# Kernel optimization log

Hardware: AMD Instinct MI355X
Metric: run time of the kernel (lower is better)

Reference implementation:

```python
import jax, jax.numpy as jnp
import numpy as np

# bitsandbytes NF4 codebook (16 quantile values in [-1, 1])
NF4 = jnp.array([
    -1.0, -0.6961928009986877, -0.5250730514526367, -0.39491748809814453,
    -0.28444138169288635, -0.18477343022823334, -0.09105003625154495, 0.0,
    0.07958029955625534, 0.16093020141124725, 0.24611230194568634,
    0.33791524171829224, 0.44070982933044434, 0.5626170039176941,
    0.7229568362236328, 1.0], dtype=jnp.float32)
BLOCK = 64  # bnb default quantization blocksize


def dequant_nf4(codes, absmax):
    """codes: int array of 4-bit indices, absmax: per-64-elem-block scale."""
    flat = NF4[codes.reshape(-1)]                      # codebook lookup
    flat = flat.reshape(-1, BLOCK) * absmax[:, None]   # per-block rescale
    return flat.reshape(codes.shape)


def setup_inputs() -> dict:
    key = jax.random.key(0)
    k1, k2, k3, k4, k5 = jax.random.split(key, 5)
    B, S, IN, OUT, R = 4, 2048, 4096, 4096, 8
    x = jax.random.normal(k1, (B, S, IN), dtype=jnp.float32)
    codes_A = jax.random.randint(k2, (R, IN), 0, 16, dtype=jnp.int32)
    absmax_A = jax.random.uniform(k3, (R * IN // BLOCK,), dtype=jnp.float32)
    codes_B = jax.random.randint(k4, (OUT, R), 0, 16, dtype=jnp.int32)
    absmax_B = jax.random.uniform(k5, (OUT * R // BLOCK,), dtype=jnp.float32)
    return {"x": x, "codes_A": codes_A, "absmax_A": absmax_A,
            "codes_B": codes_B, "absmax_B": absmax_B}


def reference(x, codes_A, absmax_A, codes_B, absmax_B):
    SCALING = 32.0 / 8.0  # alpha / rank
    W_A = dequant_nf4(codes_A, absmax_A)   # [rank, in]
    W_B = dequant_nf4(codes_B, absmax_B)   # [out, rank]
    interm = jnp.einsum('bsi,ri->bsr', x, W_A)          # lora_A: x @ W_A^T
    out = jnp.einsum('bsr,or->bso', interm, W_B)        # lora_B
    return out * SCALING
```

## Files before the change

kernel.cpp:

```cpp
#include <hip/hip_runtime.h>


static __device__ __constant__ float NF4_TBL[16] = {
    -1.0f, -0.6961928009986877f, -0.5250730514526367f, -0.39491748809814453f,
    -0.28444138169288635f, -0.18477343022823334f, -0.09105003625154495f, 0.0f,
    0.07958029955625534f, 0.16093020141124725f, 0.24611230194568634f,
    0.33791524171829224f, 0.44070982933044434f, 0.5626170039176941f,
    0.7229568362236328f, 1.0f};

__global__ void nf4_dequant_kernel(const int* __restrict__ codesA,
                                   const float* __restrict__ absA,
                                   const int* __restrict__ codesB,
                                   const float* __restrict__ absB,
                                   float* __restrict__ wA,
                                   float* __restrict__ wBt,
                                   int n) {
    int id = blockIdx.x * blockDim.x + threadIdx.x;
    if (id < n) {
        wA[id] = NF4_TBL[codesA[id] & 15] * absA[id >> 6];
        const int r = id >> 12;
        const int o = id & 4095;
        wBt[id] = NF4_TBL[codesB[o * 8 + r] & 15] * absB[o >> 3];
    }
}

__global__ __launch_bounds__(256) void lora_fused_kernel(
    const float* __restrict__ x,
    const float* __restrict__ wA,
    const float* __restrict__ wBt,
    float* __restrict__ out) {
    __shared__ float p_s[4][4][8];
    __shared__ float im_s[4][8];

    const int t    = threadIdx.x;
    const int wave = t >> 6;
    const int lane = t & 63;
    const int g    = lane >> 4;
    const int l16  = lane & 15;
    const int row0 = blockIdx.x * 4;

    const float4* __restrict__ xg =
        (const float4*)(x + (size_t)(row0 + g) * 4096) + wave * 256;
    const float4* __restrict__ wq = (const float4*)wA + wave * 256;

    float acc[8];
    #pragma unroll
    for (int r = 0; r < 8; ++r) acc[r] = 0.f;

    #pragma unroll 4
    for (int s = 0; s < 16; ++s) {
        const int idx = s * 16 + l16;
        const float4 xa = xg[idx];
        #pragma unroll
        for (int r = 0; r < 8; ++r) {
            const float4 w = wq[r * 1024 + idx];
            acc[r] += xa.x * w.x + xa.y * w.y + xa.z * w.z + xa.w * w.w;
        }
    }

    #pragma unroll
    for (int r = 0; r < 8; ++r) {
        float v = acc[r];
        #pragma unroll
        for (int off = 8; off > 0; off >>= 1) v += __shfl_down(v, off, 16);
        if (l16 == 0) p_s[wave][g][r] = v;
    }
    __syncthreads();

    if (t < 32) {
        const int m = t >> 3, r = t & 7;
        im_s[m][r] = (p_s[0][m][r] + p_s[1][m][r] +
                      p_s[2][m][r] + p_s[3][m][r]) * 4.0f;
    }
    __syncthreads();

    float ims[4][8];
    #pragma unroll
    for (int m = 0; m < 4; ++m)
        #pragma unroll
        for (int r = 0; r < 8; ++r)
            ims[m][r] = __int_as_float(
                __builtin_amdgcn_readfirstlane(__float_as_int(im_s[m][r])));

    const float4* __restrict__ wt = (const float4*)wBt;

    #pragma unroll 1
    for (int k = 0; k < 4; ++k) {
        const int og = t + 256 * k;
        float4 w[8];
        #pragma unroll
        for (int r = 0; r < 8; ++r) w[r] = wt[r * 1024 + og];

        #pragma unroll
        for (int m = 0; m < 4; ++m) {
            float4 s;
            s.x = ims[m][0] * w[0].x + ims[m][1] * w[1].x + ims[m][2] * w[2].x
                + ims[m][3] * w[3].x + ims[m][4] * w[4].x + ims[m][5] * w[5].x
                + ims[m][6] * w[6].x + ims[m][7] * w[7].x;
            s.y = ims[m][0] * w[0].y + ims[m][1] * w[1].y + ims[m][2] * w[2].y
                + ims[m][3] * w[3].y + ims[m][4] * w[4].y + ims[m][5] * w[5].y
                + ims[m][6] * w[6].y + ims[m][7] * w[7].y;
            s.z = ims[m][0] * w[0].z + ims[m][1] * w[1].z + ims[m][2] * w[2].z
                + ims[m][3] * w[3].z + ims[m][4] * w[4].z + ims[m][5] * w[5].z
                + ims[m][6] * w[6].z + ims[m][7] * w[7].z;
            s.w = ims[m][0] * w[0].w + ims[m][1] * w[1].w + ims[m][2] * w[2].w
                + ims[m][3] * w[3].w + ims[m][4] * w[4].w + ims[m][5] * w[5].w
                + ims[m][6] * w[6].w + ims[m][7] * w[7].w;
            ((float4*)(out + (size_t)(row0 + m) * 4096))[og] = s;
        }
    }
}

extern "C" void kernel_launch(void* const* d_in, const int* in_sizes, int n_in,
                              void* d_out, int out_size, void* d_ws, size_t ws_size,
                              hipStream_t stream) {
    const float* x        = (const float*)d_in[0];
    const int*   codes_A  = (const int*)d_in[1];
    const float* absmax_A = (const float*)d_in[2];
    const int*   codes_B  = (const int*)d_in[3];
    const float* absmax_B = (const float*)d_in[4];
    float* out = (float*)d_out;

    constexpr int NW = 8 * 4096;
    float* wA  = (float*)d_ws;
    float* wBt = (float*)d_ws + NW;

    nf4_dequant_kernel<<<(NW + 255) / 256, 256, 0, stream>>>(
        codes_A, absmax_A, codes_B, absmax_B, wA, wBt, NW);

    lora_fused_kernel<<<8192 / 4, 256, 0, stream>>>(x, wA, wBt, out);
}
```

Measured before the change: 268.0 us.

## Assign four rows per wave to reuse W_A loads and drop shared-memory reduction

Each wave now handles four full rows instead of the block splitting four rows across waves, so every W_A float4 load is reused across four rows. The cross-wave shared-memory reduction and the two __syncthreads are replaced by a full-wave shuffle reduction. The grid shrinks from 2048 to 512 blocks, which lowers parallelism and raises register pressure because of the 32 accumulators, while cutting redundant W_A and W_B traffic per row.

```diff
diff --git a/kernel.cpp b/kernel.cpp
--- a/kernel.cpp
+++ b/kernel.cpp
@@ -29,64 +29,61 @@
     const float* __restrict__ wA,
     const float* __restrict__ wBt,
     float* __restrict__ out) {
-    __shared__ float p_s[4][4][8];
-    __shared__ float im_s[4][8];
+    const int lane = threadIdx.x & 63;
+    const int wid  = blockIdx.x * 4 + (threadIdx.x >> 6);
+    const size_t row0 = (size_t)wid * 4;
 
-    const int t    = threadIdx.x;
-    const int wave = t >> 6;
-    const int lane = t & 63;
-    const int g    = lane >> 4;
-    const int l16  = lane & 15;
-    const int row0 = blockIdx.x * 4;
+    const float4* __restrict__ x0  = (const float4*)(x + row0 * 4096);
+    const float4* __restrict__ x1  = x0 + 1024;
+    const float4* __restrict__ x2  = x0 + 2048;
+    const float4* __restrict__ x3  = x0 + 3072;
+    const float4* __restrict__ wA4 = (const float4*)wA;
 
-    const float4* __restrict__ xg =
-        (const float4*)(x + (size_t)(row0 + g) * 4096) + wave * 256;
-    const float4* __restrict__ wq = (const float4*)wA + wave * 256;
+    float acc[4][8];
+    #pragma unroll
+    for (int m = 0; m < 4; ++m)
+        #pragma unroll
+        for (int r = 0; r < 8; ++r) acc[m][r] = 0.f;
 
-    float acc[8];
-    #pragma unroll
-    for (int r = 0; r < 8; ++r) acc[r] = 0.f;
-
-    #pragma unroll 4
-    for (int s = 0; s < 16; ++s) {
-        const int idx = s * 16 + l16;
-        const float4 xa = xg[idx];
+    #pragma unroll 1
+    for (int q = 0; q < 16; ++q) {
+        const int idx = q * 64 + lane;
+        const float4 a0 = x0[idx];
+        const float4 a1 = x1[idx];
+        const float4 a2 = x2[idx];
+        const float4 a3 = x3[idx];
         #pragma unroll
         for (int r = 0; r < 8; ++r) {
-            const float4 w = wq[r * 1024 + idx];
-            acc[r] += xa.x * w.x + xa.y * w.y + xa.z * w.z + xa.w * w.w;
+            const float4 w = wA4[r * 1024 + idx];
+            acc[0][r] += a0.x * w.x + a0.y * w.y + a0.z * w.z + a0.w * w.w;
+            acc[1][r] += a1.x * w.x + a1.y * w.y + a1.z * w.z + a1.w * w.w;
+            acc[2][r] += a2.x * w.x + a2.y * w.y + a2.z * w.z + a2.w * w.w;
+            acc[3][r] += a3.x * w.x + a3.y * w.y + a3.z * w.z + a3.w * w.w;
         }
     }
-
-    #pragma unroll
-    for (int r = 0; r < 8; ++r) {
-        float v = acc[r];
-        #pragma unroll
-        for (int off = 8; off > 0; off >>= 1) v += __shfl_down(v, off, 16);
-        if (l16 == 0) p_s[wave][g][r] = v;
-    }
-    __syncthreads();
-
-    if (t < 32) {
-        const int m = t >> 3, r = t & 7;
-        im_s[m][r] = (p_s[0][m][r] + p_s[1][m][r] +
-                      p_s[2][m][r] + p_s[3][m][r]) * 4.0f;
-    }
-    __syncthreads();
 
     float ims[4][8];
     #pragma unroll
     for (int m = 0; m < 4; ++m)
         #pragma unroll
-        for (int r = 0; r < 8; ++r)
-            ims[m][r] = __int_as_float(
-                __builtin_amdgcn_readfirstlane(__float_as_int(im_s[m][r])));
+        for (int r = 0; r < 8; ++r) {
+            float v = acc[m][r];
+            v += __shfl_down(v, 32, 64);
+            v += __shfl_down(v, 16, 64);
+            v += __shfl_down(v, 8, 64);
+            v += __shfl_down(v, 4, 64);
+            v += __shfl_down(v, 2, 64);
+            v += __shfl_down(v, 1, 64);
+            ims[m][r] = __int_as_float(__builtin_amdgcn_readfirstlane(
+                __float_as_int(v * 4.0f)));
+        }
 
     const float4* __restrict__ wt = (const float4*)wBt;
+    float4* __restrict__ o0 = (float4*)(out + row0 * 4096);
 
     #pragma unroll 1
-    for (int k = 0; k < 4; ++k) {
-        const int og = t + 256 * k;
+    for (int k = 0; k < 16; ++k) {
+        const int og = k * 64 + lane;
         float4 w[8];
         #pragma unroll
         for (int r = 0; r < 8; ++r) w[r] = wt[r * 1024 + og];
@@ -106,7 +103,7 @@
             s.w = ims[m][0] * w[0].w + ims[m][1] * w[1].w + ims[m][2] * w[2].w
                 + ims[m][3] * w[3].w + ims[m][4] * w[4].w + ims[m][5] * w[5].w
                 + ims[m][6] * w[6].w + ims[m][7] * w[7].w;
-            ((float4*)(out + (size_t)(row0 + m) * 4096))[og] = s;
+            o0[m * 1024 + og] = s;
         }
     }
 }
@@ -128,5 +125,5 @@
     nf4_dequant_kernel<<<(NW + 255) / 256, 256, 0, stream>>>(
         codes_A, absmax_A, codes_B, absmax_B, wA, wBt, NW);
 
-    lora_fused_kernel<<<8192 / 4, 256, 0, stream>>>(x, wA, wBt, out);
+    lora_fused_kernel<<<512, 256, 0, stream>>>(x, wA, wBt, out);
 }
```

Result: faster. 250.3 us (-6.6%).
